# Optimization experiments

Measured on AMD Instinct MI355X. Metric: run time of the kernel, lower is better.

Reference implementation:

```python
import jax, jax.numpy as jnp
import numpy as np

B, S, D, H = 2, 2048, 1024, 16
DH = D // H  # 64


def setup_inputs() -> dict:
    key = jax.random.key(0)
    ks = jax.random.split(key, 9)
    s = 1.0 / np.sqrt(D)
    return {
        "x": jax.random.normal(ks[0], (B, S, D), dtype=jnp.float32),
        "Wq": jax.random.normal(ks[1], (D, D), dtype=jnp.float32) * s,
        "bq": jnp.zeros((D,), dtype=jnp.float32),
        "Wk": jax.random.normal(ks[2], (D, D), dtype=jnp.float32) * s,
        "bk": jnp.zeros((D,), dtype=jnp.float32),
        "Wv": jax.random.normal(ks[3], (D, D), dtype=jnp.float32) * s,
        "bv": jnp.zeros((D,), dtype=jnp.float32),
        "Wo": jax.random.normal(ks[4], (D, D), dtype=jnp.float32) * s,
        "bo": jnp.zeros((D,), dtype=jnp.float32),
    }


def _split_heads(t):
    # [B, S, D] -> [B, H, S, DH]
    return t.reshape(B, S, H, DH).transpose(0, 2, 1, 3)


def reference(x, Wq, bq, Wk, bk, Wv, bv, Wo, bo):
    q = _split_heads(x @ Wq + bq)
    k = _split_heads(x @ Wk + bk)
    v = _split_heads(x @ Wv + bv)
    scale = 1.0 / jnp.sqrt(jnp.asarray(DH, dtype=x.dtype))
    # [B, H, S, S] score matrix (materialized, as in the original)
    logits = jnp.einsum("bhqd,bhkd->bhqk", q, k) * scale
    attn = jax.nn.softmax(logits, axis=-1)
    out = jnp.einsum("bhqk,bhkd->bhqd", attn, v)
    out = out.transpose(0, 2, 1, 3).reshape(B, S, D)
    return out @ Wo + bo
```

## Files before the change

### kernel.cpp

```cpp
#include <hip/hip_runtime.h>
#include <hip/hip_bf16.h>
#include <stdint.h>


typedef __attribute__((ext_vector_type(8))) short bf16x8;
typedef __attribute__((ext_vector_type(4))) float f32x4;

__device__ __forceinline__ void gld16(const void* g, void* l) {
  __builtin_amdgcn_global_load_lds((const __attribute__((address_space(1))) void*)g,
                                   (__attribute__((address_space(3))) void*)l, 16, 0, 0);
}

__device__ __forceinline__ unsigned short f2b(float f) {
  __hip_bfloat16 h = __float2bfloat16(f);
  return *reinterpret_cast<unsigned short*>(&h);
}

__global__ __launch_bounds__(256) void convert_x(const float* __restrict__ x,
                                                 unsigned short* __restrict__ xb) {
  int i = (blockIdx.x * 256 + threadIdx.x) * 4;
  float4 v = *(const float4*)(x + i);
  ushort4 o = make_ushort4(f2b(v.x), f2b(v.y), f2b(v.z), f2b(v.w));
  *(ushort4*)(xb + i) = o;
}

__global__ __launch_bounds__(256) void transpose_w(const float* __restrict__ Wq,
                                                   const float* __restrict__ Wk,
                                                   const float* __restrict__ Wv,
                                                   const float* __restrict__ Wo,
                                                   unsigned short* __restrict__ wt) {
  __shared__ unsigned short Ls[64 * 72];
  int z = blockIdx.z;
  const float* src = (z == 0) ? Wq : (z == 1) ? Wk : (z == 2) ? Wv : Wo;
  unsigned short* dst = wt + (size_t)z * 1024 * 1024;
  int k0 = blockIdx.x * 64, n0 = blockIdx.y * 64;
  int t = threadIdx.x;
  int c4 = t & 15;
#pragma unroll
  for (int it = 0; it < 4; ++it) {
    int row = it * 16 + (t >> 4);
    float4 v = *(const float4*)(src + (k0 + row) * 1024 + n0 + c4 * 4);
    Ls[(c4 * 4 + 0) * 72 + row] = f2b(v.x);
    Ls[(c4 * 4 + 1) * 72 + row] = f2b(v.y);
    Ls[(c4 * 4 + 2) * 72 + row] = f2b(v.z);
    Ls[(c4 * 4 + 3) * 72 + row] = f2b(v.w);
  }
  __syncthreads();
  int nr = t >> 2, kc = (t & 3) * 16;
  *(uint4*)(dst + (size_t)(n0 + nr) * 1024 + k0 + kc) = *(uint4*)&Ls[nr * 72 + kc];
  *(uint4*)(dst + (size_t)(n0 + nr) * 1024 + k0 + kc + 8) = *(uint4*)&Ls[nr * 72 + kc + 8];
}

__global__ __launch_bounds__(256) void gemm_qkv(const unsigned short* __restrict__ Ab,
                                                const unsigned short* __restrict__ Bt,
                                                const float* __restrict__ bq,
                                                const float* __restrict__ bk,
                                                const float* __restrict__ bv,
                                                unsigned short* __restrict__ qb,
                                                unsigned short* __restrict__ kb,
                                                unsigned short* __restrict__ vtb) {
  __shared__ unsigned short As[128 * 32];
  __shared__ unsigned short Bs[128 * 32];
  const int t = threadIdx.x;
  const int lane = t & 63, wave = t >> 6;
  const int m0 = blockIdx.x * 128, n0 = blockIdx.y * 128;
  const int wr = (wave >> 1) * 64, wc = (wave & 1) * 64;
  const int fr = lane & 15, fq = lane >> 4;
  f32x4 acc[4][4] = {};
  for (int kt = 0; kt < 32; ++kt) {
    const unsigned short* Ag = Ab + (size_t)m0 * 1024 + kt * 32;
    const unsigned short* Bg = Bt + (size_t)n0 * 1024 + kt * 32;
#pragma unroll
    for (int rep = 0; rep < 2; ++rep) {
      int c = t + rep * 256;
      int row = c >> 2, col = (c & 3) * 8;
      gld16(Ag + (size_t)row * 1024 + col, (void*)(As + c * 8));
      gld16(Bg + (size_t)row * 1024 + col, (void*)(Bs + c * 8));
    }
    __syncthreads();
    bf16x8 a[4], b[4];
#pragma unroll
    for (int i = 0; i < 4; ++i) a[i] = *(const bf16x8*)&As[(wr + i * 16 + fr) * 32 + fq * 8];
#pragma unroll
    for (int j = 0; j < 4; ++j) b[j] = *(const bf16x8*)&Bs[(wc + j * 16 + fr) * 32 + fq * 8];
#pragma unroll
    for (int i = 0; i < 4; ++i)
#pragma unroll
      for (int j = 0; j < 4; ++j)
        acc[i][j] = __builtin_amdgcn_mfma_f32_16x16x32_bf16(a[i], b[j], acc[i][j], 0, 0, 0);
    __syncthreads();
  }
  int which = n0 >> 10;
  if (which == 2) {
#pragma unroll
    for (int j = 0; j < 4; ++j) {
      int gn = n0 + wc + j * 16 + fr;
      int nl = gn & 1023, h = nl >> 6, dh = nl & 63;
      float bias = bv[nl];
#pragma unroll
      for (int i = 0; i < 4; ++i) {
        int s0 = m0 + wr + i * 16 + fq * 4;
        int bidx = s0 >> 11, s = s0 & 2047;
        ushort4 pk;
        pk.x = f2b(acc[i][j][0] + bias);
        pk.y = f2b(acc[i][j][1] + bias);
        pk.z = f2b(acc[i][j][2] + bias);
        pk.w = f2b(acc[i][j][3] + bias);
        *(uint2*)&vtb[(size_t)((bidx * 16 + h) * 64 + dh) * 2048 + s] = *(uint2*)&pk;
      }
    }
  } else {
    unsigned short* dst = (which == 0) ? qb : kb;
    const float* bias_p = (which == 0) ? bq : bk;
    float scale = (which == 0) ? 0.1803368801111204f : 1.0f;
#pragma unroll
    for (int j = 0; j < 4; ++j) {
      int gn = n0 + wc + j * 16 + fr;
      int nl = gn & 1023, h = nl >> 6, dh = nl & 63;
      float bias = bias_p[nl];
#pragma unroll
      for (int i = 0; i < 4; ++i) {
#pragma unroll
        for (int r = 0; r < 4; ++r) {
          int gm = m0 + wr + i * 16 + fq * 4 + r;
          int bidx = gm >> 11, s = gm & 2047;
          dst[(size_t)((bidx * 16 + h) * 2048 + s) * 64 + dh] = f2b((acc[i][j][r] + bias) * scale);
        }
      }
    }
  }
}

__global__ __launch_bounds__(256, 2) void attn_kernel(const unsigned short* __restrict__ qb,
                                                      const unsigned short* __restrict__ kb,
                                                      const unsigned short* __restrict__ vtb,
                                                      unsigned short* __restrict__ attn) {
  __shared__ unsigned short Ks[2 * 4096];
  __shared__ unsigned short Vs[2 * 4096];
  __shared__ unsigned short Ps[4 * 2048];
  const int t = threadIdx.x, lane = t & 63, w = t >> 6;
  const int fr = lane & 15, fq = lane >> 4;
  const int bh = blockIdx.y, q0 = blockIdx.x * 128;
  const unsigned short* qg = qb + (size_t)bh * 2048 * 64;
  const unsigned short* kg0 = kb + (size_t)bh * 2048 * 64;
  const unsigned short* vg0 = vtb + (size_t)bh * 64 * 2048;

  bf16x8 qf[2][2];
#pragma unroll
  for (int nb = 0; nb < 2; ++nb)
#pragma unroll
    for (int kk = 0; kk < 2; ++kk)
      qf[nb][kk] = *(const bf16x8*)(qg + (size_t)(q0 + w * 32 + nb * 16 + fr) * 64 + kk * 32 + fq * 8);

  bf16x8 ones;
#pragma unroll
  for (int i = 0; i < 8; ++i) ones[i] = (short)0x3F80;

  f32x4 oacc[2][4] = {};
  f32x4 lacc[2] = {};
  unsigned short* Pw = Ps + w * 2048;
  const int swz = fr & 7;

  {
    const unsigned short* kg = kg0;
    const unsigned short* vg = vg0;
#pragma unroll
    for (int rep = 0; rep < 2; ++rep) {
      int c = t + rep * 256;
      int kk = c >> 8, row = (c >> 2) & 63, cc = c & 3;
      gld16(kg + row * 64 + kk * 32 + cc * 8, (void*)(Ks + c * 8));
      gld16(vg + (size_t)row * 2048 + kk * 32 + cc * 8, (void*)(Vs + c * 8));
    }
  }

  for (int kt = 0; kt < 32; ++kt) {
    int buf = kt & 1;
    __syncthreads();
    if (kt + 1 < 32) {
      const unsigned short* kg = kg0 + (size_t)(kt + 1) * 4096;
      const unsigned short* vg = vg0 + (kt + 1) * 64;
      int lb = (buf ^ 1) * 4096;
#pragma unroll
      for (int rep = 0; rep < 2; ++rep) {
        int c = t + rep * 256;
        int kk = c >> 8, row = (c >> 2) & 63, cc = c & 3;
        gld16(kg + row * 64 + kk * 32 + cc * 8, (void*)(Ks + lb + c * 8));
        gld16(vg + (size_t)row * 2048 + kk * 32 + cc * 8, (void*)(Vs + lb + c * 8));
      }
    }
    const unsigned short* Kb = Ks + buf * 4096;
    const unsigned short* Vb = Vs + buf * 4096;
    f32x4 sacc[4][2] = {};
#pragma unroll
    for (int kk = 0; kk < 2; ++kk) {
      bf16x8 kf[4];
#pragma unroll
      for (int m = 0; m < 4; ++m) kf[m] = *(const bf16x8*)&Kb[kk * 2048 + (m * 16 + fr) * 32 + fq * 8];
#pragma unroll
      for (int m = 0; m < 4; ++m)
#pragma unroll
        for (int nb = 0; nb < 2; ++nb)
          sacc[m][nb] = __builtin_amdgcn_mfma_f32_16x16x32_bf16(kf[m], qf[nb][kk], sacc[m][nb], 0, 0, 0);
    }
#pragma unroll
    for (int m = 0; m < 4; ++m)
#pragma unroll
      for (int nb = 0; nb < 2; ++nb) {
        int qw = nb * 16 + fr;
        int G = (m * 2 + (fq >> 1)) ^ (qw & 7);
        ushort4 pk;
        pk.x = f2b(__builtin_amdgcn_exp2f(sacc[m][nb][0]));
        pk.y = f2b(__builtin_amdgcn_exp2f(sacc[m][nb][1]));
        pk.z = f2b(__builtin_amdgcn_exp2f(sacc[m][nb][2]));
        pk.w = f2b(__builtin_amdgcn_exp2f(sacc[m][nb][3]));
        *(uint2*)&Pw[qw * 64 + G * 8 + (fq & 1) * 4] = *(uint2*)&pk;
      }
#pragma unroll
    for (int kk = 0; kk < 2; ++kk) {
      bf16x8 pf[2];
#pragma unroll
      for (int mb = 0; mb < 2; ++mb) {
        int qw = mb * 16 + fr;
        int G = (kk * 4 + fq) ^ (qw & 7);
        pf[mb] = *(const bf16x8*)&Pw[qw * 64 + G * 8];
      }
#pragma unroll
      for (int n = 0; n < 4; ++n) {
        bf16x8 vf = *(const bf16x8*)&Vb[kk * 2048 + (n * 16 + fr) * 32 + fq * 8];
#pragma unroll
        for (int mb = 0; mb < 2; ++mb)
          oacc[mb][n] = __builtin_amdgcn_mfma_f32_16x16x32_bf16(pf[mb], vf, oacc[mb][n], 0, 0, 0);
      }
#pragma unroll
      for (int mb = 0; mb < 2; ++mb)
        lacc[mb] = __builtin_amdgcn_mfma_f32_16x16x32_bf16(pf[mb], ones, lacc[mb], 0, 0, 0);
    }
  }
  int bidx = bh >> 4, h = bh & 15;
#pragma unroll
  for (int mb = 0; mb < 2; ++mb)
#pragma unroll
    for (int r = 0; r < 4; ++r) {
      float inv = 1.f / lacc[mb][r];
      int s = q0 + w * 32 + mb * 16 + fq * 4 + r;
      size_t base = (size_t)(bidx * 2048 + s) * 1024 + h * 64;
#pragma unroll
      for (int n = 0; n < 4; ++n) attn[base + n * 16 + fr] = f2b(oacc[mb][n][r] * inv);
    }
}

__global__ __launch_bounds__(256) void gemm_out(const unsigned short* __restrict__ Ab,
                                                const unsigned short* __restrict__ Bt,
                                                const float* __restrict__ bo,
                                                float* __restrict__ out) {
  __shared__ unsigned short As[128 * 32];
  __shared__ unsigned short Bs[128 * 32];
  const int t = threadIdx.x;
  const int lane = t & 63, wave = t >> 6;
  const int m0 = blockIdx.x * 128, n0 = blockIdx.y * 128;
  const int wr = (wave >> 1) * 64, wc = (wave & 1) * 64;
  const int fr = lane & 15, fq = lane >> 4;
  f32x4 acc[4][4] = {};
  for (int kt = 0; kt < 32; ++kt) {
    const unsigned short* Ag = Ab + (size_t)m0 * 1024 + kt * 32;
    const unsigned short* Bg = Bt + (size_t)n0 * 1024 + kt * 32;
#pragma unroll
    for (int rep = 0; rep < 2; ++rep) {
      int c = t + rep * 256;
      int row = c >> 2, col = (c & 3) * 8;
      gld16(Ag + (size_t)row * 1024 + col, (void*)(As + c * 8));
      gld16(Bg + (size_t)row * 1024 + col, (void*)(Bs + c * 8));
    }
    __syncthreads();
    bf16x8 a[4], b[4];
#pragma unroll
    for (int i = 0; i < 4; ++i) a[i] = *(const bf16x8*)&As[(wr + i * 16 + fr) * 32 + fq * 8];
#pragma unroll
    for (int j = 0; j < 4; ++j) b[j] = *(const bf16x8*)&Bs[(wc + j * 16 + fr) * 32 + fq * 8];
#pragma unroll
    for (int i = 0; i < 4; ++i)
#pragma unroll
      for (int j = 0; j < 4; ++j)
        acc[i][j] = __builtin_amdgcn_mfma_f32_16x16x32_bf16(a[i], b[j], acc[i][j], 0, 0, 0);
    __syncthreads();
  }
#pragma unroll
  for (int j = 0; j < 4; ++j) {
    int gn = n0 + wc + j * 16 + fr;
    float bias = bo[gn];
#pragma unroll
    for (int i = 0; i < 4; ++i)
#pragma unroll
      for (int r = 0; r < 4; ++r) {
        int gm = m0 + wr + i * 16 + fq * 4 + r;
        out[(size_t)gm * 1024 + gn] = acc[i][j][r] + bias;
      }
  }
}

extern "C" void kernel_launch(void* const* d_in, const int* in_sizes, int n_in,
                              void* d_out, int out_size, void* d_ws, size_t ws_size,
                              hipStream_t stream) {
  const float* x = (const float*)d_in[0];
  const float* Wq = (const float*)d_in[1];
  const float* bq = (const float*)d_in[2];
  const float* Wk = (const float*)d_in[3];
  const float* bk = (const float*)d_in[4];
  const float* Wv = (const float*)d_in[5];
  const float* bv = (const float*)d_in[6];
  const float* Wo = (const float*)d_in[7];
  const float* bo = (const float*)d_in[8];
  float* out = (float*)d_out;

  unsigned short* ws = (unsigned short*)d_ws;
  const size_t MI = (size_t)1024 * 1024;
  unsigned short* xb = ws;
  unsigned short* wt = ws + 4 * MI;
  unsigned short* qb = wt + 4 * MI;
  unsigned short* kb = qb + 4 * MI;
  unsigned short* vtb = kb + 4 * MI;
  unsigned short* attn = xb;

  convert_x<<<4096, 256, 0, stream>>>(x, xb);
  transpose_w<<<dim3(16, 16, 4), 256, 0, stream>>>(Wq, Wk, Wv, Wo, wt);
  gemm_qkv<<<dim3(32, 24), 256, 0, stream>>>(xb, wt, bq, bk, bv, qb, kb, vtb);
  attn_kernel<<<dim3(16, 32), 256, 0, stream>>>(qb, kb, vtb, attn);
  gemm_out<<<dim3(32, 8), 256, 0, stream>>>(attn, wt + 3 * MI, bo, out);
}
```

Baseline: 209.6 us.

## Stage QKV epilogue through LDS for coalesced stores; merge prep kernels

```diff
diff --git a/kernel.cpp b/kernel.cpp
--- a/kernel.cpp
+++ b/kernel.cpp
@@ -16,25 +16,29 @@
   return *reinterpret_cast<unsigned short*>(&h);
 }
 
-__global__ __launch_bounds__(256) void convert_x(const float* __restrict__ x,
-                                                 unsigned short* __restrict__ xb) {
-  int i = (blockIdx.x * 256 + threadIdx.x) * 4;
-  float4 v = *(const float4*)(x + i);
-  ushort4 o = make_ushort4(f2b(v.x), f2b(v.y), f2b(v.z), f2b(v.w));
-  *(ushort4*)(xb + i) = o;
-}
-
-__global__ __launch_bounds__(256) void transpose_w(const float* __restrict__ Wq,
+__global__ __launch_bounds__(256) void prep_kernel(const float* __restrict__ x,
+                                                   const float* __restrict__ Wq,
                                                    const float* __restrict__ Wk,
                                                    const float* __restrict__ Wv,
                                                    const float* __restrict__ Wo,
+                                                   unsigned short* __restrict__ xb,
                                                    unsigned short* __restrict__ wt) {
   __shared__ unsigned short Ls[64 * 72];
-  int z = blockIdx.z;
+  int bid = blockIdx.x;
+  int t = threadIdx.x;
+  if (bid < 4096) {
+    int i = (bid * 256 + t) * 4;
+    float4 v = *(const float4*)(x + i);
+    ushort4 o = make_ushort4(f2b(v.x), f2b(v.y), f2b(v.z), f2b(v.w));
+    *(ushort4*)(xb + i) = o;
+    return;
+  }
+  int tid = bid - 4096;
+  int z = tid >> 8, rem = tid & 255;
+  int bx = rem & 15, by = rem >> 4;
   const float* src = (z == 0) ? Wq : (z == 1) ? Wk : (z == 2) ? Wv : Wo;
   unsigned short* dst = wt + (size_t)z * 1024 * 1024;
-  int k0 = blockIdx.x * 64, n0 = blockIdx.y * 64;
-  int t = threadIdx.x;
+  int k0 = bx * 64, n0 = by * 64;
   int c4 = t & 15;
 #pragma unroll
   for (int it = 0; it < 4; ++it) {
@@ -61,6 +65,7 @@
                                                 unsigned short* __restrict__ vtb) {
   __shared__ unsigned short As[128 * 32];
   __shared__ unsigned short Bs[128 * 32];
+  __shared__ unsigned short Es[128 * 72];
   const int t = threadIdx.x;
   const int lane = t & 63, wave = t >> 6;
   const int m0 = blockIdx.x * 128, n0 = blockIdx.y * 128;
@@ -90,43 +95,69 @@
         acc[i][j] = __builtin_amdgcn_mfma_f32_16x16x32_bf16(a[i], b[j], acc[i][j], 0, 0, 0);
     __syncthreads();
   }
-  int which = n0 >> 10;
+  const int which = n0 >> 10;
+  const int bidx = m0 >> 11, s0 = m0 & 2047;
   if (which == 2) {
 #pragma unroll
-    for (int j = 0; j < 4; ++j) {
-      int gn = n0 + wc + j * 16 + fr;
-      int nl = gn & 1023, h = nl >> 6, dh = nl & 63;
-      float bias = bv[nl];
-#pragma unroll
-      for (int i = 0; i < 4; ++i) {
-        int s0 = m0 + wr + i * 16 + fq * 4;
-        int bidx = s0 >> 11, s = s0 & 2047;
-        ushort4 pk;
-        pk.x = f2b(acc[i][j][0] + bias);
-        pk.y = f2b(acc[i][j][1] + bias);
-        pk.z = f2b(acc[i][j][2] + bias);
-        pk.w = f2b(acc[i][j][3] + bias);
-        *(uint2*)&vtb[(size_t)((bidx * 16 + h) * 64 + dh) * 2048 + s] = *(uint2*)&pk;
-      }
+    for (int nh = 0; nh < 2; ++nh) {
+      if ((wc >> 6) == nh) {
+#pragma unroll
+        for (int j = 0; j < 4; ++j) {
+          int col = j * 16 + fr;
+          float bias = bv[(n0 + nh * 64 + col) & 1023];
+#pragma unroll
+          for (int i = 0; i < 4; ++i) {
+            int sl = wr + i * 16 + fq * 4;
+            ushort4 pk;
+            pk.x = f2b(acc[i][j][0] + bias);
+            pk.y = f2b(acc[i][j][1] + bias);
+            pk.z = f2b(acc[i][j][2] + bias);
+            pk.w = f2b(acc[i][j][3] + bias);
+            *(uint2*)&Es[col * 136 + sl] = *(uint2*)&pk;
+          }
+        }
+      }
+      __syncthreads();
+      int h = ((n0 + nh * 64) & 1023) >> 6;
+#pragma unroll
+      for (int it = 0; it < 4; ++it) {
+        int dh = it * 16 + (t >> 4);
+        int ck = (t & 15) * 8;
+        uint4 vv = *(uint4*)&Es[dh * 136 + ck];
+        *(uint4*)&vtb[(size_t)((bidx * 16 + h) * 64 + dh) * 2048 + s0 + ck] = vv;
+      }
+      __syncthreads();
     }
   } else {
     unsigned short* dst = (which == 0) ? qb : kb;
     const float* bias_p = (which == 0) ? bq : bk;
     float scale = (which == 0) ? 0.1803368801111204f : 1.0f;
 #pragma unroll
-    for (int j = 0; j < 4; ++j) {
-      int gn = n0 + wc + j * 16 + fr;
-      int nl = gn & 1023, h = nl >> 6, dh = nl & 63;
-      float bias = bias_p[nl];
-#pragma unroll
-      for (int i = 0; i < 4; ++i) {
-#pragma unroll
-        for (int r = 0; r < 4; ++r) {
-          int gm = m0 + wr + i * 16 + fq * 4 + r;
-          int bidx = gm >> 11, s = gm & 2047;
-          dst[(size_t)((bidx * 16 + h) * 2048 + s) * 64 + dh] = f2b((acc[i][j][r] + bias) * scale);
+    for (int nh = 0; nh < 2; ++nh) {
+      if ((wc >> 6) == nh) {
+#pragma unroll
+        for (int j = 0; j < 4; ++j) {
+          int col = j * 16 + fr;
+          float bias = bias_p[(n0 + nh * 64 + col) & 1023];
+#pragma unroll
+          for (int i = 0; i < 4; ++i)
+#pragma unroll
+            for (int r = 0; r < 4; ++r) {
+              int sl = wr + i * 16 + fq * 4 + r;
+              Es[sl * 72 + col] = f2b((acc[i][j][r] + bias) * scale);
+            }
         }
       }
+      __syncthreads();
+      int h = ((n0 + nh * 64) & 1023) >> 6;
+#pragma unroll
+      for (int it = 0; it < 4; ++it) {
+        int sl = it * 32 + (t >> 3);
+        int ck = (t & 7) * 8;
+        uint4 vv = *(uint4*)&Es[sl * 72 + ck];
+        *(uint4*)&dst[(size_t)((bidx * 16 + h) * 2048 + s0 + sl) * 64 + ck] = vv;
+      }
+      __syncthreads();
     }
   }
 }
@@ -159,17 +190,14 @@
   f32x4 oacc[2][4] = {};
   f32x4 lacc[2] = {};
   unsigned short* Pw = Ps + w * 2048;
-  const int swz = fr & 7;
 
   {
-    const unsigned short* kg = kg0;
-    const unsigned short* vg = vg0;
 #pragma unroll
     for (int rep = 0; rep < 2; ++rep) {
       int c = t + rep * 256;
       int kk = c >> 8, row = (c >> 2) & 63, cc = c & 3;
-      gld16(kg + row * 64 + kk * 32 + cc * 8, (void*)(Ks + c * 8));
-      gld16(vg + (size_t)row * 2048 + kk * 32 + cc * 8, (void*)(Vs + c * 8));
+      gld16(kg0 + row * 64 + kk * 32 + cc * 8, (void*)(Ks + c * 8));
+      gld16(vg0 + (size_t)row * 2048 + kk * 32 + cc * 8, (void*)(Vs + c * 8));
     }
   }
 
@@ -321,8 +349,7 @@
   unsigned short* vtb = kb + 4 * MI;
   unsigned short* attn = xb;
 
-  convert_x<<<4096, 256, 0, stream>>>(x, xb);
-  transpose_w<<<dim3(16, 16, 4), 256, 0, stream>>>(Wq, Wk, Wv, Wo, wt);
+  prep_kernel<<<5120, 256, 0, stream>>>(x, Wq, Wk, Wv, Wo, xb, wt);
   gemm_qkv<<<dim3(32, 24), 256, 0, stream>>>(xb, wt, bq, bk, bv, qb, kb, vtb);
   attn_kernel<<<dim3(16, 32), 256, 0, stream>>>(qb, kb, vtb, attn);
   gemm_out<<<dim3(32, 8), 256, 0, stream>>>(attn, wt + 3 * MI, bo, out);
```

New measurement: 209.3 us. No clear change (-0.1%).
